# Optimization experiments

Hardware: AMD Instinct MI355X
Metric: run time of the kernel (lower is better)

Reference implementation:

```python
import jax, jax.numpy as jnp
import numpy as np

N_COARSE = 100_000
M_FINE = 4 * N_COARSE
GRID = 128
C_IN, C_HID, C_OUT = 32, 64, 32
K3 = 27   # 3x3x3 neighborhood
K2 = 8    # 2x2x2 transposed-conv offsets


def setup_inputs() -> dict:
    rng = np.random.default_rng(0)
    # --- sparse coarse grid: N unique voxels in GRID^3 ---
    lin = np.sort(rng.choice(GRID ** 3, size=N_COARSE, replace=False))
    cx, cy, cz = lin // (GRID * GRID), (lin // GRID) % GRID, lin % GRID
    coords = np.stack([cx, cy, cz], 1).astype(np.int64)
    # --- rulebook: neighbor index per voxel per 3^3 offset (sentinel = N) ---
    offs = np.array([(dx, dy, dz) for dx in (-1, 0, 1) for dy in (-1, 0, 1) for dz in (-1, 0, 1)])
    nbr = np.full((N_COARSE, K3), N_COARSE, np.int32)
    for k in range(K3):
        nc = coords + offs[k]
        valid = ((nc >= 0) & (nc < GRID)).all(1)
        nlin = nc[:, 0] * GRID * GRID + nc[:, 1] * GRID + nc[:, 2]
        pos = np.clip(np.searchsorted(lin, nlin), 0, N_COARSE - 1)
        found = valid & (lin[pos] == nlin)
        nbr[found, k] = pos[found].astype(np.int32)
    # --- fine grid: 4 distinct children (of 8) per coarse voxel ---
    child = np.argsort(rng.random((N_COARSE, K2)), axis=1)[:, :4].astype(np.int32)
    parent_idx = np.repeat(np.arange(N_COARSE, dtype=np.int32), 4)
    offset_idx = child.reshape(-1)

    key = jax.random.key(0)
    ks = jax.random.split(key, 16)
    nrm = lambda k, sh, fan: (jax.random.normal(k, sh, jnp.float32) / np.sqrt(fan)).astype(jnp.float32)
    return {
        "feats_in": jax.random.normal(ks[0], (N_COARSE, C_IN), jnp.float32),
        "x_up_feats": jax.random.normal(ks[1], (M_FINE, C_OUT), jnp.float32),
        "nbr_idx": jnp.asarray(nbr),
        "parent_idx": jnp.asarray(parent_idx),
        "offset_idx": jnp.asarray(offset_idx),
        "W_enc1": nrm(ks[2], (K3, C_IN, C_HID), K3 * C_IN),
        "b_enc1": jnp.zeros((C_HID,), jnp.float32),
        "W_enc2": nrm(ks[3], (K3, C_HID, C_HID), K3 * C_HID),
        "b_enc2": jnp.zeros((C_HID,), jnp.float32),
        "W_enc3": nrm(ks[4], (K3, C_HID, C_HID), K3 * C_HID),
        "b_enc3": jnp.zeros((C_HID,), jnp.float32),
        "W_t": nrm(ks[5], (K2, C_HID, C_HID), C_HID),
        "b_t": jnp.zeros((C_HID,), jnp.float32),
        "W_d1": nrm(ks[6], (C_HID, C_HID), C_HID),
        "b_d1": jnp.zeros((C_HID,), jnp.float32),
        "W_d2": nrm(ks[7], (C_HID, C_OUT), C_HID),
        "b_d2": jnp.zeros((C_OUT,), jnp.float32),
    }


def _sparse_conv3(x, nbr, W, b):
    """3x3x3 stride-1 sparse conv: gather neighbors, per-offset matmul, accumulate.
    x: [N,Cin], nbr: [N,27] (sentinel N -> zero feature), W: [27,Cin,Cout]."""
    xp = jnp.concatenate([x, jnp.zeros((1, x.shape[1]), x.dtype)], 0)  # sentinel row
    acc = jnp.broadcast_to(b, (x.shape[0], W.shape[-1]))
    for k in range(W.shape[0]):  # fixed 27-way structural loop
        acc = acc + xp[nbr[:, k]] @ W[k]
    return acc


def _t_conv2(x, parent_idx, offset_idx, W, b):
    """2x2x2 stride-2 transposed sparse conv onto a given fine grid.
    x: [N,C], parent_idx: [M] (sentinel N), offset_idx: [M] in [0,8)."""
    xp = jnp.concatenate([x, jnp.zeros((1, x.shape[1]), x.dtype)], 0)
    g = xp[parent_idx]  # [M,C]
    out = jnp.broadcast_to(b, (g.shape[0], W.shape[-1]))
    for k in range(W.shape[0]):  # fixed 8-way structural loop
        out = out + jnp.where((offset_idx == k)[:, None], g @ W[k], 0.0)
    return out


def reference(feats_in, x_up_feats, nbr_idx, parent_idx, offset_idx,
              W_enc1, b_enc1, W_enc2, b_enc2, W_enc3, b_enc3,
              W_t, b_t, W_d1, b_d1, W_d2, b_d2):
    # encoder: (conv -> dropout[eval: identity] -> relu) x 3
    x = jax.nn.relu(_sparse_conv3(feats_in, nbr_idx, W_enc1, b_enc1))
    x = jax.nn.relu(_sparse_conv3(x, nbr_idx, W_enc2, b_enc2))
    x = jax.nn.relu(_sparse_conv3(x, nbr_idx, W_enc3, b_enc3))
    # transposed upsample conv onto x_upsample's grid
    x = _t_conv2(x, parent_idx, offset_idx, W_t, b_t)
    # decoder: relu -> 1x1 conv -> relu -> 1x1 conv, then residual add
    x = jax.nn.relu(x) @ W_d1 + b_d1
    x = jax.nn.relu(x) @ W_d2 + b_d2
    return x + x_up_feats
```

## Files before the change

kernel.cpp:

```cpp
#include <hip/hip_runtime.h>
#include <hip/hip_bf16.h>

#define NC 100000
#define MF 400000
#define K3 27

typedef __bf16 bf16_t;
typedef bf16_t bf16x8 __attribute__((ext_vector_type(8)));
typedef float  f32x4  __attribute__((ext_vector_type(4)));

#define O_E1 0
#define O_E2 55296
#define O_E3 165888
#define O_T  276480
#define O_D1 309248
#define O_D2 313344
#define W_TOTAL 315392

__device__ __align__(16) bf16_t g_w[W_TOTAL];
__device__ __align__(16) bf16_t g_x0[(size_t)NC * 32];
__device__ __align__(16) bf16_t g_x1[(size_t)NC * 64];
__device__ __align__(16) bf16_t g_x2[(size_t)NC * 64];
__device__ int g_nbrT[(size_t)K3 * NC];

static __device__ __forceinline__ bf16x8 zero8() {
    bf16x8 v;
#pragma unroll
    for (int i = 0; i < 8; ++i) v[i] = (bf16_t)0.0f;
    return v;
}

__global__ __launch_bounds__(256) void prep_k(
    const float* __restrict__ W_e1, const float* __restrict__ W_e2,
    const float* __restrict__ W_e3, const float* __restrict__ W_t,
    const float* __restrict__ W_d1, const float* __restrict__ W_d2,
    const float* __restrict__ feats, const int* __restrict__ nbr)
{
    int b = blockIdx.x;
    if (b < 154) {
        int tid = b * 256 + threadIdx.x;
        int lane = tid & 63;
        int f = tid >> 6;
        const float* src; int doff, nt, nc, fb;
        if      (f < 108) { src = W_e1; doff = O_E1; nt = 4; nc = 1; fb = 0;   }
        else if (f < 324) { src = W_e2; doff = O_E2; nt = 4; nc = 2; fb = 108; }
        else if (f < 540) { src = W_e3; doff = O_E3; nt = 4; nc = 2; fb = 324; }
        else if (f < 604) { src = W_t;  doff = O_T;  nt = 4; nc = 2; fb = 540; }
        else if (f < 612) { src = W_d1; doff = O_D1; nt = 4; nc = 2; fb = 604; }
        else              { src = W_d2; doff = O_D2; nt = 2; nc = 2; fb = 612; }
        int lf = f - fb;
        int t  = lf % nt;
        int c  = (lf / nt) % nc;
        int ko = lf / (nt * nc);
        int Cin = nc * 32, Cout = nt * 16;
        int n  = t * 16 + (lane & 15);
        int kb = c * 32 + (lane >> 4) * 8;
        bf16x8 tmp;
#pragma unroll
        for (int j = 0; j < 8; ++j)
            tmp[j] = (bf16_t)src[((size_t)ko * Cin + (kb + j)) * Cout + n];
        *(bf16x8*)(g_w + doff + (size_t)lf * 512 + lane * 8) = tmp;
    } else if (b < 1717) {
        int i = (b - 154) * 256 + threadIdx.x;
        if (i < NC * 32 / 8) {
            const f32x4* p = (const f32x4*)(feats + (size_t)i * 8);
            f32x4 lo = p[0], hi = p[1];
            bf16x8 v;
#pragma unroll
            for (int j = 0; j < 4; ++j) { v[j] = (bf16_t)lo[j]; v[j + 4] = (bf16_t)hi[j]; }
            *(bf16x8*)(g_x0 + (size_t)i * 8) = v;
        }
    } else {
        int r = (b - 1717) * 256 + threadIdx.x;
        if (r < NC) {
#pragma unroll
            for (int k = 0; k < K3; ++k)
                g_nbrT[(size_t)k * NC + r] = nbr[(size_t)r * K3 + k];
        }
    }
}

#define TS 72

#define CSTEP(KO, P) do {                                                      \
    if ((KO) + 1 < K3) {                                                       \
                            \
        const bf16x8* s_ = (const bf16x8*)(wsrc + (size_t)((KO) + 1) * CH * 2048); \
        bf16x8* d_ = (bf16x8*)bB[(P) ^ 1];                                     \
        _Pragma("unroll")                                                      \
        for (int i_ = 0; i_ < CH * 2; ++i_)                                    \
            d_[i_ * 128 + tid] = s_[i_ * 128 + tid];                           \
                 \
        _Pragma("unroll")                                                      \
        for (int c_ = 0; c_ < CH; ++c_)                                        \
            _Pragma("unroll")                                                  \
            for (int mt_ = 0; mt_ < 4; ++mt_) {                                \
                int ii_ = idxbuf[(P) ^ 1][mt_];                                \
                bool va_ = (unsigned)ii_ < (unsigned)NC;                       \
                int ss_ = va_ ? ii_ : 0;                                       \
                bf16x8 a_ = *(const bf16x8*)(xb + (size_t)ss_ * CIN + c_ * 32 + q * 8); \
                if (!va_) a_ = zero8();                                        \
                abuf[(P) ^ 1][c_][mt_] = a_;                                   \
            }                                                                  \
    }                                                                          \
    if ((KO) + 2 < K3) {                                                       \
                 \
        _Pragma("unroll")                                                      \
        for (int mt_ = 0; mt_ < 4; ++mt_) {                                    \
            int r_ = base + mt_ * 16 + cl;                                     \
            idxbuf[P][mt_] = (r_ < NC) ? g_nbrT[(size_t)((KO) + 2) * NC + r_] : NC; \
        }                                                                      \
    }                                                                          \
                                        \
    _Pragma("unroll")                                                          \
    for (int c_ = 0; c_ < CH; ++c_) {                                          \
        bf16x8 bfr_[4];                                                        \
        _Pragma("unroll")                                                      \
        for (int t_ = 0; t_ < 4; ++t_)                                         \
            bfr_[t_] = *(const bf16x8*)&bB[P][(c_ * 4 + t_) * 512 + lane * 8]; \
        _Pragma("unroll")                                                      \
        for (int mt_ = 0; mt_ < 4; ++mt_)                                      \
            _Pragma("unroll")                                                  \
            for (int t_ = 0; t_ < 4; ++t_)                                     \
                acc[mt_][t_] = __builtin_amdgcn_mfma_f32_16x16x32_bf16(        \
                    abuf[P][c_][mt_], bfr_[t_], acc[mt_][t_], 0, 0, 0);        \
    }                                                                          \
    __syncthreads();                                                           \
} while (0)

template <int CH>
__global__ __launch_bounds__(128, 1) void conv_k(
    int w_off,
    const float* __restrict__ bias,
    int src_sel, int dst_sel)
{
    constexpr int CIN = CH * 32;
    const bf16_t* xb = (src_sel == 0) ? g_x0 : (src_sel == 1 ? g_x1 : g_x2);
    bf16_t* y = (dst_sel == 1) ? g_x1 : g_x2;
    const bf16_t* wsrc = g_w + w_off;

    __shared__ __align__(16) bf16_t bB[2][4096];
    int tid = threadIdx.x;
    int wv = tid >> 6, lane = tid & 63;
    int cl = lane & 15, q = lane >> 4;

    int per = gridDim.x >> 3;
    int blk = (blockIdx.x & 7) * per + (blockIdx.x >> 3);
    int base = (blk * 2 + wv) * 64;

    {
        const bf16x8* s = (const bf16x8*)wsrc;
        bf16x8* d = (bf16x8*)bB[0];
#pragma unroll
        for (int i = 0; i < CH * 2; ++i) d[i * 128 + tid] = s[i * 128 + tid];
    }

    int idxbuf[2][4];
    bf16x8 abuf[2][CH][4];
#pragma unroll
    for (int mt = 0; mt < 4; ++mt) {
        int r = base + mt * 16 + cl;
        idxbuf[0][mt] = (r < NC) ? g_nbrT[(size_t)0 * NC + r] : NC;
    }
#pragma unroll
    for (int c = 0; c < CH; ++c)
#pragma unroll
        for (int mt = 0; mt < 4; ++mt) {
            int ii = idxbuf[0][mt];
            bool va = (unsigned)ii < (unsigned)NC;
            int ss = va ? ii : 0;
            bf16x8 a = *(const bf16x8*)(xb + (size_t)ss * CIN + c * 32 + q * 8);
            if (!va) a = zero8();
            abuf[0][c][mt] = a;
        }
#pragma unroll
    for (int mt = 0; mt < 4; ++mt) {
        int r = base + mt * 16 + cl;
        idxbuf[1][mt] = (r < NC) ? g_nbrT[(size_t)1 * NC + r] : NC;
    }

    f32x4 acc[4][4];
#pragma unroll
    for (int t = 0; t < 4; ++t) {
        float b = bias[t * 16 + cl];
#pragma unroll
        for (int mt = 0; mt < 4; ++mt) acc[mt][t] = (f32x4){b, b, b, b};
    }
    __syncthreads();

    for (int ko = 0; ko < K3 - 1; ko += 2) {
        CSTEP(ko, 0);
        CSTEP(ko + 1, 1);
    }
    CSTEP(K3 - 1, 0);

    bf16_t* tb = ((bf16_t*)bB) + wv * 2304;
#pragma unroll
    for (int ch = 0; ch < 2; ++ch) {
#pragma unroll
        for (int mt2 = 0; mt2 < 2; ++mt2)
#pragma unroll
            for (int t = 0; t < 4; ++t)
#pragma unroll
                for (int r = 0; r < 4; ++r) {
                    float v = acc[ch * 2 + mt2][t][r];
                    v = v > 0.0f ? v : 0.0f;
                    tb[(mt2 * 16 + q * 4 + r) * TS + t * 16 + cl] = (bf16_t)v;
                }
#pragma unroll
        for (int i = 0; i < 4; ++i) {
            int rl = i * 8 + (lane >> 3);
            int c8 = (lane & 7) * 8;
            bf16x8 v8 = *(const bf16x8*)&tb[rl * TS + c8];
            int orow = base + ch * 32 + rl;
            if (orow < NC)
                *(bf16x8*)(y + (size_t)orow * 64 + c8) = v8;
        }
    }
}

#define HS 72
__global__ __launch_bounds__(256) void tconv_dec_k(
    const int*   __restrict__ offs,
    const float* __restrict__ b_t,
    const float* __restrict__ b_d1,
    const float* __restrict__ b_d2,
    const float* __restrict__ x_up,
    float*       __restrict__ out)
{
    __shared__ __align__(16) bf16_t h_lds[4][64 * HS];
    __shared__ __align__(16) int off_lds[4][64];
    int wv = threadIdx.x >> 6, lane = threadIdx.x & 63;
    int cl = lane & 15, q = lane >> 4;
    int per = gridDim.x >> 3;
    int blk = (blockIdx.x & 7) * per + (blockIdx.x >> 3);
    int p0 = (blk * 4 + wv) * 16;
    int fbase = p0 * 4;

    f32x4 xup[8];
#pragma unroll
    for (int i = 0; i < 8; ++i) {
        int rl = i * 8 + (lane >> 3);
        int c4 = (lane & 7) * 4;
        int fg = fbase + rl;
        if (fg < MF) xup[i] = *(const f32x4*)(x_up + (size_t)fg * 32 + c4);
        else         xup[i] = (f32x4){0.f, 0.f, 0.f, 0.f};
    }

    {
        int fi = fbase + lane;
        off_lds[wv][lane] = (fi < MF) ? offs[fi] : 0;
    }
    int code[4];
#pragma unroll
    for (int r = 0; r < 4; ++r) {
        int4 o = *(const int4*)&off_lds[wv][(q * 4 + r) * 4];
        code[r] = (1 << (4 * o.x)) | (2 << (4 * o.y)) |
                  (3 << (4 * o.z)) | (4 << (4 * o.w));
    }

    bool pv = (p0 + cl) < NC;
    size_t xrow = (size_t)(pv ? p0 + cl : 0) * 64;
    bf16x8 ax[2];
#pragma unroll
    for (int c = 0; c < 2; ++c) {
        bf16x8 t8 = *(const bf16x8*)(g_x1 + xrow + c * 32 + q * 8);
        ax[c] = pv ? t8 : zero8();
    }

    const bf16_t* wt = g_w + O_T;
#pragma unroll
    for (int k = 0; k < 8; ++k) {
        f32x4 acc[4];
#pragma unroll
        for (int t = 0; t < 4; ++t) {
            float b = b_t[t * 16 + cl];
            acc[t] = (f32x4){b, b, b, b};
        }
#pragma unroll
        for (int c = 0; c < 2; ++c) {
            const bf16_t* wb = wt + ((size_t)(k * 2 + c) * 4) * 512 + lane * 8;
#pragma unroll
            for (int t = 0; t < 4; ++t) {
                bf16x8 b = *(const bf16x8*)(wb + t * 512);
                acc[t] = __builtin_amdgcn_mfma_f32_16x16x32_bf16(ax[c], b, acc[t], 0, 0, 0);
            }
        }
#pragma unroll
        for (int r = 0; r < 4; ++r) {
            int nib = (code[r] >> (4 * k)) & 0xF;
            if (nib) {
                int fl = (((q * 4 + r) * 4) + (nib - 1)) & 63;
#pragma unroll
                for (int t = 0; t < 4; ++t) {
                    float v = acc[t][r];
                    v = v > 0.0f ? v : 0.0f;
                    h_lds[wv][fl * HS + t * 16 + cl] = (bf16_t)v;
                }
            }
        }
    }

    bf16x8 a1[4][2];
#pragma unroll
    for (int mt = 0; mt < 4; ++mt)
#pragma unroll
        for (int c = 0; c < 2; ++c)
            a1[mt][c] = *(const bf16x8*)&h_lds[wv][(mt * 16 + cl) * HS + c * 32 + q * 8];

#pragma unroll
    for (int mt = 0; mt < 4; ++mt) {
        f32x4 acc2[4];
#pragma unroll
        for (int t = 0; t < 4; ++t) {
            float b = b_d1[t * 16 + cl];
            acc2[t] = (f32x4){b, b, b, b};
        }
#pragma unroll
        for (int c = 0; c < 2; ++c)
#pragma unroll
            for (int t = 0; t < 4; ++t) {
                bf16x8 b = *(const bf16x8*)(g_w + O_D1 + (size_t)(c * 4 + t) * 512 + lane * 8);
                acc2[t] = __builtin_amdgcn_mfma_f32_16x16x32_bf16(a1[mt][c], b, acc2[t], 0, 0, 0);
            }
#pragma unroll
        for (int t = 0; t < 4; ++t)
#pragma unroll
            for (int r = 0; r < 4; ++r) {
                float v = acc2[t][r];
                v = v > 0.0f ? v : 0.0f;
                h_lds[wv][(mt * 16 + q * 4 + r) * HS + t * 16 + cl] = (bf16_t)v;
            }
    }

    float* fW = (float*)h_lds[wv];
#pragma unroll
    for (int mt = 0; mt < 4; ++mt) {
        bf16x8 a2[2];
#pragma unroll
        for (int c = 0; c < 2; ++c)
            a2[c] = *(const bf16x8*)&h_lds[wv][(mt * 16 + cl) * HS + c * 32 + q * 8];
        f32x4 acc3[2];
#pragma unroll
        for (int t = 0; t < 2; ++t) {
            float b = b_d2[t * 16 + cl];
            acc3[t] = (f32x4){b, b, b, b};
        }
#pragma unroll
        for (int c = 0; c < 2; ++c)
#pragma unroll
            for (int t = 0; t < 2; ++t) {
                bf16x8 b = *(const bf16x8*)(g_w + O_D2 + (size_t)(c * 2 + t) * 512 + lane * 8);
                acc3[t] = __builtin_amdgcn_mfma_f32_16x16x32_bf16(a2[c], b, acc3[t], 0, 0, 0);
            }
#pragma unroll
        for (int t = 0; t < 2; ++t)
#pragma unroll
            for (int r = 0; r < 4; ++r)
                fW[(mt * 16 + q * 4 + r) * 36 + t * 16 + cl] = acc3[t][r];
    }

#pragma unroll
    for (int i = 0; i < 8; ++i) {
        int rl = i * 8 + (lane >> 3);
        int c4 = (lane & 7) * 4;
        int fg = fbase + rl;
        if (fg < MF) {
            f32x4 v = *(const f32x4*)&fW[rl * 36 + c4];
            v += xup[i];
            *(f32x4*)(out + (size_t)fg * 32 + c4) = v;
        }
    }
}

extern "C" void kernel_launch(void* const* d_in, const int* in_sizes, int n_in,
                              void* d_out, int out_size, void* d_ws, size_t ws_size,
                              hipStream_t stream) {
    const float* feats  = (const float*)d_in[0];
    const float* x_up   = (const float*)d_in[1];
    const int*   nbr    = (const int*)d_in[2];
    const int*   offs   = (const int*)d_in[4];
    const float* W_e1 = (const float*)d_in[5];
    const float* b_e1 = (const float*)d_in[6];
    const float* W_e2 = (const float*)d_in[7];
    const float* b_e2 = (const float*)d_in[8];
    const float* W_e3 = (const float*)d_in[9];
    const float* b_e3 = (const float*)d_in[10];
    const float* W_t  = (const float*)d_in[11];
    const float* b_t  = (const float*)d_in[12];
    const float* W_d1 = (const float*)d_in[13];
    const float* b_d1 = (const float*)d_in[14];
    const float* W_d2 = (const float*)d_in[15];
    const float* b_d2 = (const float*)d_in[16];
    float* out = (float*)d_out;

    prep_k<<<2108, 256, 0, stream>>>(W_e1, W_e2, W_e3, W_t, W_d1, W_d2, feats, nbr);

    conv_k<1><<<784, 128, 0, stream>>>(O_E1, b_e1, 0, 1);
    conv_k<2><<<784, 128, 0, stream>>>(O_E2, b_e2, 1, 2);
    conv_k<2><<<784, 128, 0, stream>>>(O_E3, b_e3, 2, 1);

    tconv_dec_k<<<1568, 256, 0, stream>>>(offs, b_t, b_d1, b_d2, x_up, out);
}
```

Measured before the change: 337.8 us.

## Load conv weights directly into registers, single-wave blocks, drop LDS staging and barriers

The sparse conv kernel no longer stages each offset's weight slice into shared memory with block barriers. Each single-wave block now loads its MFMA B fragments straight from global (L2-cached) memory into double-buffered registers. The transposed-conv/decoder kernel moves to 2-wave blocks and loads x_up just before the residual add instead of prefetching it, which frees registers. This removes __syncthreads stalls and LDS traffic, at the cost of more register pressure and repeated global weight reads per wave.

```diff
diff --git a/kernel.cpp b/kernel.cpp
--- a/kernel.cpp
+++ b/kernel.cpp
@@ -82,15 +82,17 @@
 
 #define TS 72
 
-#define CSTEP(KO, P) do {                                                      \
+#define KSTEP(KO, P) do {                                                      \
     if ((KO) + 1 < K3) {                                                       \
-                            \
-        const bf16x8* s_ = (const bf16x8*)(wsrc + (size_t)((KO) + 1) * CH * 2048); \
-        bf16x8* d_ = (bf16x8*)bB[(P) ^ 1];                                     \
+                                \
+        const bf16_t* wb_ = wsrc + (size_t)((KO) + 1) * CH * 2048 + lane * 8;  \
         _Pragma("unroll")                                                      \
-        for (int i_ = 0; i_ < CH * 2; ++i_)                                    \
-            d_[i_ * 128 + tid] = s_[i_ * 128 + tid];                           \
-                 \
+        for (int c_ = 0; c_ < CH; ++c_)                                        \
+            _Pragma("unroll")                                                  \
+            for (int t_ = 0; t_ < 4; ++t_)                                     \
+                bbuf[(P) ^ 1][c_][t_] =                                        \
+                    *(const bf16x8*)(wb_ + (size_t)(c_ * 4 + t_) * 512);       \
+                         \
         _Pragma("unroll")                                                      \
         for (int c_ = 0; c_ < CH; ++c_)                                        \
             _Pragma("unroll")                                                  \
@@ -104,32 +106,26 @@
             }                                                                  \
     }                                                                          \
     if ((KO) + 2 < K3) {                                                       \
-                 \
+                     \
         _Pragma("unroll")                                                      \
         for (int mt_ = 0; mt_ < 4; ++mt_) {                                    \
             int r_ = base + mt_ * 16 + cl;                                     \
             idxbuf[P][mt_] = (r_ < NC) ? g_nbrT[(size_t)((KO) + 2) * NC + r_] : NC; \
         }                                                                      \
     }                                                                          \
-                                        \
+                                       \
     _Pragma("unroll")                                                          \
-    for (int c_ = 0; c_ < CH; ++c_) {                                          \
-        bf16x8 bfr_[4];                                                        \
-        _Pragma("unroll")                                                      \
-        for (int t_ = 0; t_ < 4; ++t_)                                         \
-            bfr_[t_] = *(const bf16x8*)&bB[P][(c_ * 4 + t_) * 512 + lane * 8]; \
+    for (int c_ = 0; c_ < CH; ++c_)                                            \
         _Pragma("unroll")                                                      \
         for (int mt_ = 0; mt_ < 4; ++mt_)                                      \
             _Pragma("unroll")                                                  \
             for (int t_ = 0; t_ < 4; ++t_)                                     \
                 acc[mt_][t_] = __builtin_amdgcn_mfma_f32_16x16x32_bf16(        \
-                    abuf[P][c_][mt_], bfr_[t_], acc[mt_][t_], 0, 0, 0);        \
-    }                                                                          \
-    __syncthreads();                                                           \
+                    abuf[P][c_][mt_], bbuf[P][c_][t_], acc[mt_][t_], 0, 0, 0); \
 } while (0)
 
 template <int CH>
-__global__ __launch_bounds__(128, 1) void conv_k(
+__global__ __launch_bounds__(64, 1) void conv_k(
     int w_off,
     const float* __restrict__ bias,
     int src_sel, int dst_sel)
@@ -139,28 +135,30 @@
     bf16_t* y = (dst_sel == 1) ? g_x1 : g_x2;
     const bf16_t* wsrc = g_w + w_off;
 
-    __shared__ __align__(16) bf16_t bB[2][4096];
-    int tid = threadIdx.x;
-    int wv = tid >> 6, lane = tid & 63;
+    __shared__ __align__(16) bf16_t tb[2304];
+    int lane = threadIdx.x & 63;
     int cl = lane & 15, q = lane >> 4;
 
     int per = gridDim.x >> 3;
     int blk = (blockIdx.x & 7) * per + (blockIdx.x >> 3);
-    int base = (blk * 2 + wv) * 64;
-
-    {
-        const bf16x8* s = (const bf16x8*)wsrc;
-        bf16x8* d = (bf16x8*)bB[0];
-#pragma unroll
-        for (int i = 0; i < CH * 2; ++i) d[i * 128 + tid] = s[i * 128 + tid];
-    }
+    int base = blk * 64;
 
     int idxbuf[2][4];
     bf16x8 abuf[2][CH][4];
+    bf16x8 bbuf[2][CH][4];
+
 #pragma unroll
     for (int mt = 0; mt < 4; ++mt) {
         int r = base + mt * 16 + cl;
         idxbuf[0][mt] = (r < NC) ? g_nbrT[(size_t)0 * NC + r] : NC;
+    }
+    {
+        const bf16_t* wb = wsrc + lane * 8;
+#pragma unroll
+        for (int c = 0; c < CH; ++c)
+#pragma unroll
+            for (int t = 0; t < 4; ++t)
+                bbuf[0][c][t] = *(const bf16x8*)(wb + (size_t)(c * 4 + t) * 512);
     }
 #pragma unroll
     for (int c = 0; c < CH; ++c)
@@ -186,15 +184,13 @@
 #pragma unroll
         for (int mt = 0; mt < 4; ++mt) acc[mt][t] = (f32x4){b, b, b, b};
     }
-    __syncthreads();
 
     for (int ko = 0; ko < K3 - 1; ko += 2) {
-        CSTEP(ko, 0);
-        CSTEP(ko + 1, 1);
-    }
-    CSTEP(K3 - 1, 0);
-
-    bf16_t* tb = ((bf16_t*)bB) + wv * 2304;
+        KSTEP(ko, 0);
+        KSTEP(ko + 1, 1);
+    }
+    KSTEP(K3 - 1, 0);
+
 #pragma unroll
     for (int ch = 0; ch < 2; ++ch) {
 #pragma unroll
@@ -220,7 +216,7 @@
 }
 
 #define HS 72
-__global__ __launch_bounds__(256) void tconv_dec_k(
+__global__ __launch_bounds__(128) void tconv_dec_k(
     const int*   __restrict__ offs,
     const float* __restrict__ b_t,
     const float* __restrict__ b_d1,
@@ -228,24 +224,14 @@
     const float* __restrict__ x_up,
     float*       __restrict__ out)
 {
-    __shared__ __align__(16) bf16_t h_lds[4][64 * HS];
-    __shared__ __align__(16) int off_lds[4][64];
+    __shared__ __align__(16) bf16_t h_lds[2][64 * HS];
+    __shared__ __align__(16) int off_lds[2][64];
     int wv = threadIdx.x >> 6, lane = threadIdx.x & 63;
     int cl = lane & 15, q = lane >> 4;
     int per = gridDim.x >> 3;
     int blk = (blockIdx.x & 7) * per + (blockIdx.x >> 3);
-    int p0 = (blk * 4 + wv) * 16;
+    int p0 = (blk * 2 + wv) * 16;
     int fbase = p0 * 4;
-
-    f32x4 xup[8];
-#pragma unroll
-    for (int i = 0; i < 8; ++i) {
-        int rl = i * 8 + (lane >> 3);
-        int c4 = (lane & 7) * 4;
-        int fg = fbase + rl;
-        if (fg < MF) xup[i] = *(const f32x4*)(x_up + (size_t)fg * 32 + c4);
-        else         xup[i] = (f32x4){0.f, 0.f, 0.f, 0.f};
-    }
 
     {
         int fi = fbase + lane;
@@ -366,8 +352,9 @@
         int c4 = (lane & 7) * 4;
         int fg = fbase + rl;
         if (fg < MF) {
+            f32x4 xv = *(const f32x4*)(x_up + (size_t)fg * 32 + c4);
             f32x4 v = *(const f32x4*)&fW[rl * 36 + c4];
-            v += xup[i];
+            v += xv;
             *(f32x4*)(out + (size_t)fg * 32 + c4) = v;
         }
     }
@@ -396,9 +383,9 @@
 
     prep_k<<<2108, 256, 0, stream>>>(W_e1, W_e2, W_e3, W_t, W_d1, W_d2, feats, nbr);
 
-    conv_k<1><<<784, 128, 0, stream>>>(O_E1, b_e1, 0, 1);
-    conv_k<2><<<784, 128, 0, stream>>>(O_E2, b_e2, 1, 2);
-    conv_k<2><<<784, 128, 0, stream>>>(O_E3, b_e3, 2, 1);
-
-    tconv_dec_k<<<1568, 256, 0, stream>>>(offs, b_t, b_d1, b_d2, x_up, out);
-}
+    conv_k<1><<<1568, 64, 0, stream>>>(O_E1, b_e1, 0, 1);
+    conv_k<2><<<1568, 64, 0, stream>>>(O_E2, b_e2, 1, 2);
+    conv_k<2><<<1568, 64, 0, stream>>>(O_E3, b_e3, 2, 1);
+
+    tconv_dec_k<<<3128, 128, 0, stream>>>(offs, b_t, b_d1, b_d2, x_up, out);
+}
```

After: 343.2 us. Within noise of the previous version (+1.6%).
